# Performance work log

Hardware: AMD Instinct MI355X
Metric: run time of the kernel (lower is better)

Reference implementation:

```python
import jax, jax.numpy as jnp
import numpy as np

EPS = 1e-4
SLOPE = 0.01
NFFT = 512
HOP = 256
CH_IN = 8
CH_H = 64
FREQ = NFFT // 2 + 1
LEN = 48000
BATCH = 2


def hann(n):
    return (0.5 - 0.5 * jnp.cos(2.0 * np.pi * jnp.arange(n) / n)).astype(jnp.float32)


def stft(x):
    # x: (B, C, L) -> (B, 2, C, F, T)  (torch.stft: center=True, reflect pad, hann window)
    pad = NFFT // 2
    xp = jnp.pad(x, ((0, 0), (0, 0), (pad, pad)), mode='reflect')
    T = 1 + x.shape[-1] // HOP
    idx = jnp.arange(T)[:, None] * HOP + jnp.arange(NFFT)[None, :]
    frames = xp[..., idx] * hann(NFFT)            # (B, C, T, NFFT)
    sp = jnp.fft.rfft(frames, axis=-1)            # (B, C, T, F)
    sp = jnp.swapaxes(sp, -1, -2)                 # (B, C, F, T)
    return jnp.stack([sp.real, sp.imag], axis=1).astype(jnp.float32)


def istft(re, im, length):
    # re, im: (B, C, F, T) -> (B, C, length) via windowed overlap-add
    sp = jnp.swapaxes(re + 1j * im, -1, -2)       # (B, C, T, F)
    win = hann(NFFT)
    frames = jnp.fft.irfft(sp, n=NFFT, axis=-1) * win
    pad = NFFT // 2
    total = length + 2 * pad
    T = frames.shape[-2]
    idx = jnp.arange(T)[:, None] * HOP + jnp.arange(NFFT)[None, :]
    out = jnp.zeros(frames.shape[:-2] + (total,), frames.dtype).at[..., idx].add(frames)
    wsum = jnp.zeros((total,), frames.dtype).at[idx].add(jnp.broadcast_to(win ** 2, (T, NFFT)))
    return (out / jnp.maximum(wsum, 1e-11))[..., pad:pad + length]


def conv2d(x, w, b, padT=0):
    y = jax.lax.conv_general_dilated(x, w, (1, 1), ((0, 0), (padT, padT)),
                                     dimension_numbers=('NCHW', 'OIHW', 'NCHW'))
    return y + b[None, :, None, None]


def cconv(x, w, b, padT=0):
    # complex conv on x: (B,2,C,F,T); w: (2,O,C,kf,kt) = [W_real, W_imag]; b: (2,O)
    r = conv2d(x[:, 0], w[0], b[0], padT) - conv2d(x[:, 1], w[1], b[1], padT)
    i = conv2d(x[:, 1], w[0], b[0], padT) + conv2d(x[:, 0], w[1], b[1], padT)
    return jnp.stack([r, i], axis=1)


def modExp(x, m=5.0):
    em = float(np.exp(m))
    return jnp.where(x > m, (x - m) * em + em, jnp.exp(jnp.minimum(x, m)))


def cExp(t):
    e = modExp(t[:, 0]) - 1.0
    return jnp.stack([e * jnp.cos(t[:, 1] - 1.0), e * jnp.sin(t[:, 1] - 1.0)], axis=1)


def snap(x):
    x = jnp.where((x >= 0) & (x < EPS), EPS, x)
    return jnp.where((x < 0) & (x > -EPS), -EPS, x)


def cLog(t):
    re = snap(t[:, 0])
    im = snap(t[:, 1])
    real = jnp.log(jnp.sqrt(im ** 2 + re ** 2 + EPS ** 2) + 1.0)
    imag = jnp.arctan(im / re)
    return jnp.stack([real, imag], axis=1)


def cMul(a, b):
    r = a[:, 0] * b[:, 0] - a[:, 1] * b[:, 1]
    i = a[:, 0] * b[:, 1] + a[:, 1] * b[:, 0]
    return jnp.stack([r, i], axis=1)


def trelu(t, tr, b):
    nr = t[:, 0] * tr[0, 0] + t[:, 1] * tr[0, 1] + b[0]
    ni = t[:, 0] * tr[1, 0] + t[:, 1] * tr[1, 1] + b[1]
    return jnp.stack([jax.nn.leaky_relu(nr, SLOPE), jax.nn.leaky_relu(ni, SLOPE)], axis=1)


def tgate(t, tr, b):
    gr = jax.nn.sigmoid(t[:, 0] * tr[0, 0] + t[:, 1] * tr[0, 1] + b[0])
    gi = jax.nn.sigmoid(t[:, 0] * tr[1, 0] + t[:, 1] * tr[1, 1] + b[1])
    return gr * gi + (1.0 - gr) * (1.0 - gi)


def perm(t):
    return jnp.transpose(t, (0, 1, 3, 2, 4))


def lrelu(x):
    return jax.nn.leaky_relu(x, SLOPE)


def forward(mix, fs_w, fs_b, fr_w, fr_b, c1r_w, c1r_b, c1i_w, c1i_b, c1_w, c1_b,
            c2r_w, c2r_b, c2i_w, c2i_b, c2_w, c2_b, a1_t, a1_b, a2_t, a2_b,
            c3r_w, c3r_b, c3i_w, c3i_b, c3_w, c3_b, c4r_w, c4r_b, c4i_w, c4i_b,
            c4_w, c4_b, a3_t, a3_b, a4_t, a4_b, f1_w, f1_b, f2_w, f2_b,
            cw_w, cw_b, fg_t, fg_b):
    ts = perm(cconv(perm(stft(mix)), fs_w, fs_b))      # (B,2,C,F,T)
    # ---- branch 1 ----
    tl = cLog(ts)
    tl = jnp.stack([conv2d(tl[:, 0], c1r_w, c1r_b), conv2d(tl[:, 1], c1r_w, c1r_b)], 1)
    tl = jnp.stack([conv2d(lrelu(tl[:, 0]), c1i_w, c1i_b), conv2d(tl[:, 1], c1i_w, c1i_b)], 1)
    tl = trelu(cExp(tl), a1_t, a1_b)
    t = cconv(tl, c1_w, c1_b)
    tl = cLog(t)
    tl = jnp.stack([conv2d(tl[:, 0], c2r_w, c2r_b, 7), conv2d(tl[:, 1], c2r_w, c2r_b, 7)], 1)[..., :-7]
    tl = jnp.stack([conv2d(lrelu(tl[:, 0]), c2i_w, c2i_b, 7), conv2d(tl[:, 1], c2i_w, c2i_b, 7)], 1)[..., :-7]
    tl = cExp(tl)
    tl1 = tl
    tc = cconv(ts, c2_w, c2_b, 7)[..., :-7]
    t = trelu(cMul(tl, tc), a2_t, a2_b)
    t = cconv(t, f1_w, f1_b)
    td1 = jnp.sum(ts - t, axis=2, keepdims=True) / ts.shape[2]
    # ---- branch 2 ----
    tl = cLog(ts)
    tl = jnp.stack([conv2d(tl[:, 0], c3r_w, c3r_b), conv2d(tl[:, 1], c3r_w, c3r_b)], 1)
    tl = jnp.stack([conv2d(lrelu(tl[:, 0]), c3i_w, c3i_b), conv2d(tl[:, 1], c3i_w, c3i_b)], 1)
    tl = trelu(cExp(tl), a3_t, a3_b)
    t = cconv(tl, c3_w, c3_b)
    tl = cLog(t)
    tl = jnp.stack([conv2d(tl[:, 0], c4r_w, c4r_b, 7), conv2d(tl[:, 1], c4r_w, c4r_b, 7)], 1)[..., :-7]
    tl = jnp.stack([conv2d(lrelu(tl[:, 0]), c4i_w, c4i_b, 7), conv2d(tl[:, 1], c4i_w, c4i_b, 7)], 1)[..., :-7]
    tl = cExp(tl)
    tc = cconv(ts, c4_w, c4_b, 7)[..., :-7]
    t = trelu(cMul(tl, tc), a4_t, a4_b)
    td2 = cconv(t, f2_w, f2_b)                         # (B,2,1,F,T)
    # ---- fuse ----
    f = cconv(jnp.concatenate([tl1, tl], axis=2), cw_w, cw_b)
    f = tgate(f, fg_t, fg_b)[:, None]                  # (B,1,1,F,T)
    td = td1 * f + td2 * (1.0 - f)
    t = perm(cconv(perm(td), fr_w, fr_b))
    return istft(t[:, 0], t[:, 1], LEN)                # (B,1,LEN)


def setup_inputs() -> dict:
    ks = iter(jax.random.split(jax.random.key(0), 64))
    def rn(shape, s=0.05):
        return s * jax.random.normal(next(ks), shape, jnp.float32)
    F, C, H = FREQ, CH_IN, CH_H
    inp = {
        'mix': jax.random.normal(next(ks), (BATCH, C, LEN), jnp.float32),
        'fs_w': rn((2, F, F, 1, 1)), 'fs_b': rn((2, F), 0.01),
        'fr_w': rn((2, F, F, 1, 1)), 'fr_b': rn((2, F), 0.01),
        'c1r_w': rn((H, C, 1, 1)), 'c1r_b': rn((H,), 0.01),
        'c1i_w': rn((H, H, 1, 1)), 'c1i_b': rn((H,), 0.01),
        'c1_w': rn((2, H, H, 1, 1)), 'c1_b': rn((2, H), 0.01),
        'c2r_w': rn((H, H, 1, 8)), 'c2r_b': rn((H,), 0.01),
        'c2i_w': rn((H, H, 1, 8)), 'c2i_b': rn((H,), 0.01),
        'c2_w': rn((2, H, C, 1, 8)), 'c2_b': rn((2, H), 0.01),
        'a1_t': rn((2, 2, H, F, 1), 0.5), 'a1_b': rn((2, H, F, 1), 0.5),
        'a2_t': rn((2, 2, H, F, 1), 0.5), 'a2_b': rn((2, H, F, 1), 0.5),
        'c3r_w': rn((H, C, 1, 1)), 'c3r_b': rn((H,), 0.01),
        'c3i_w': rn((H, H, 1, 1)), 'c3i_b': rn((H,), 0.01),
        'c3_w': rn((2, H, H, 1, 1)), 'c3_b': rn((2, H), 0.01),
        'c4r_w': rn((H, H, 1, 8)), 'c4r_b': rn((H,), 0.01),
        'c4i_w': rn((H, H, 1, 8)), 'c4i_b': rn((H,), 0.01),
        'c4_w': rn((2, H, C, 1, 8)), 'c4_b': rn((2, H), 0.01),
        'a3_t': rn((2, 2, H, F, 1), 0.5), 'a3_b': rn((2, H, F, 1), 0.5),
        'a4_t': rn((2, 2, H, F, 1), 0.5), 'a4_b': rn((2, H, F, 1), 0.5),
        'f1_w': rn((2, C, H, 1, 1)), 'f1_b': rn((2, C), 0.01),
        'f2_w': rn((2, 1, H, 1, 1)), 'f2_b': rn((2, 1), 0.01),
        'cw_w': rn((2, 1, 2 * H, 1, 1)), 'cw_b': rn((2, 1), 0.01),
        'fg_t': rn((2, 2, 1, F, 1), 0.5), 'fg_b': rn((2, 1, F, 1), 0.5),
    }
    return inp


def reference(mix, fs_w, fs_b, fr_w, fr_b, c1r_w, c1r_b, c1i_w, c1i_b, c1_w, c1_b,
              c2r_w, c2r_b, c2i_w, c2i_b, c2_w, c2_b, a1_t, a1_b, a2_t, a2_b,
              c3r_w, c3r_b, c3i_w, c3i_b, c3_w, c3_b, c4r_w, c4r_b, c4i_w, c4i_b,
              c4_w, c4_b, a3_t, a3_b, a4_t, a4_b, f1_w, f1_b, f2_w, f2_b,
              cw_w, cw_b, fg_t, fg_b):
    return forward(mix, fs_w, fs_b, fr_w, fr_b, c1r_w, c1r_b, c1i_w, c1i_b, c1_w, c1_b,
                   c2r_w, c2r_b, c2i_w, c2i_b, c2_w, c2_b, a1_t, a1_b, a2_t, a2_b,
                   c3r_w, c3r_b, c3i_w, c3i_b, c3_w, c3_b, c4r_w, c4r_b, c4i_w, c4i_b,
                   c4_w, c4_b, a3_t, a3_b, a4_t, a4_b, f1_w, f1_b, f2_w, f2_b,
                   cw_w, cw_b, fg_t, fg_b)
```

## Files before the change

kernel.cpp:

```cpp
#include <hip/hip_runtime.h>
#include <math.h>

#define DEV __device__ __forceinline__

constexpr int B_   = 2;
constexpr int C_IN = 8;
constexpr int H_   = 64;
constexpr int F_   = 257;
constexpr int T_   = 188;
constexpr int TW   = 96;
constexpr int NFFT = 512;
constexpr int HOP  = 256;
constexpr int LEN  = 48000;
constexpr int PADL = 256;
constexpr int FT   = F_ * T_;
constexpr float EPSV  = 1e-4f;
constexpr float SLOPEV = 0.01f;
constexpr float PI2 = 6.283185307179586f;

typedef __attribute__((ext_vector_type(8))) short short8;
typedef __attribute__((ext_vector_type(4))) float float4v;

DEV float lrelu_f(float x) { return x > 0.f ? x : SLOPEV * x; }
DEV float snap_f(float x) {
  if (x >= 0.f && x < EPSV) return EPSV;
  if (x < 0.f && x > -EPSV) return -EPSV;
  return x;
}
DEV float modexp_f(float x) {
  const float em = 148.4131591025766f;
  return x > 5.f ? (x - 5.f) * em + em : expf(x);
}
DEV void cexp_f(float tr, float ti, float& er, float& ei) {
  float e = modexp_f(tr) - 1.f;
  float s, c;
  sincosf(ti - 1.f, &s, &c);
  er = e * c; ei = e * s;
}
DEV float sigmoid_f(float x) { return 1.f / (1.f + expf(-x)); }

DEV short f2bf(float x) {
  unsigned u = __float_as_uint(x);
  unsigned r = (u + 0x7fffu + ((u >> 16) & 1u)) >> 16;
  return (short)r;
}
DEV float bf2f(short h) {
  return __uint_as_float(((unsigned)(unsigned short)h) << 16);
}

__global__ __launch_bounds__(320) void k_stft(const float* __restrict__ mix,
                                              float* __restrict__ out) {
  __shared__ float xw[NFFT], xu[256], xv[256];
  int blk = blockIdx.x;
  int t = blk % T_;
  int bc = blk / T_;
  int c = bc % C_IN;
  int b = bc / C_IN;
  int tid = threadIdx.x;
  for (int n = tid; n < NFFT; n += 320) {
    int g = t * HOP + n - PADL;
    if (g < 0) g = -g;
    if (g >= LEN) g = 2 * LEN - 2 - g;
    float win = 0.5f - 0.5f * cosf((PI2 / NFFT) * n);
    xw[n] = mix[(b * C_IN + c) * LEN + g] * win;
  }
  __syncthreads();
  for (int n = tid + 1; n < 256; n += 320) {
    xu[n] = xw[n] + xw[NFFT - n];
    xv[n] = xw[n] - xw[NFFT - n];
  }
  __syncthreads();
  int f = tid;
  if (f < F_) {
    float sd, cd;
    sincosf((PI2 / NFFT) * f, &sd, &cd);
    float cs = cd, sn = sd, re = 0.f, im = 0.f;
    for (int n = 1; n < 256; ++n) {
      re += xu[n] * cs;
      im -= xv[n] * sn;
      float t2 = cs * cd - sn * sd;
      sn = sn * cd + cs * sd;
      cs = t2;
    }
    re += xw[0] + xw[256] * (1.f - 2.f * (f & 1));
    out[((b * 2 + 0) * C_IN + c) * FT + f * T_ + t] = re;
    out[((b * 2 + 1) * C_IN + c) * FT + f * T_ + t] = im;
  }
}

template<int CH>
__global__ void k_fmix(const float* __restrict__ X, const float* __restrict__ W,
                       const float* __restrict__ bias, float* __restrict__ Y) {
  int fo = blockIdx.x;
  int bc = blockIdx.y; int c = bc % CH; int b = bc / CH;
  int t = threadIdx.x;
  if (t >= T_) return;
  const float* wr = W + fo * F_;
  const float* wi = W + F_ * F_ + fo * F_;
  const float* xr = X + ((b * 2 + 0) * CH + c) * FT + t;
  const float* xi = X + ((b * 2 + 1) * CH + c) * FT + t;
  float ar = 0.f, ai = 0.f;
  for (int fi = 0; fi < F_; ++fi) {
    float wrv = wr[fi], wiv = wi[fi];
    float xrv = xr[fi * T_], xiv = xi[fi * T_];
    ar += wrv * xrv - wiv * xiv;
    ai += wrv * xiv + wiv * xrv;
  }
  float br = bias[fo], bi = bias[F_ + fo];
  Y[((b * 2 + 0) * CH + c) * FT + fo * T_ + t] = ar + br - bi;
  Y[((b * 2 + 1) * CH + c) * FT + fo * T_ + t] = ai + br + bi;
}

template<int CIN, int K>
DEV void repack_real_body(const float* __restrict__ W, short* __restrict__ wpk, int i) {
  constexpr int CC = (CIN >= 32) ? (CIN / 32) : 1;
  constexpr int NSTEP = (CIN * K + 31) / 32;
  int total = 2 * NSTEP * 4 * 64 * 8;
  if (i >= total) return;
  int j = i & 7;
  int lane = (i >> 3) & 63;
  int mt = (i >> 9) & 3;
  int s = (i >> 11) % NSTEP;
  int split = i / (NSTEP * 2048);
  int q = lane >> 4;
  int m = mt * 16 + (lane & 15);
  int tap = s / CC;
  int c = (s % CC) * 32 + q * 8 + j;
  float w = 0.f;
  if (c < CIN && tap < K) w = W[(m * CIN + c) * K + tap];
  short hi = f2bf(w);
  wpk[i] = split ? f2bf(w - bf2f(hi)) : hi;
}

template<int CIN2, int COUT2, int K>
DEV void repack_cplx_body(const float* __restrict__ W, short* __restrict__ wpk, int i) {
  constexpr int CIN = CIN2 / 2, COUT = COUT2 / 2;
  constexpr int NSTEP = CIN2 * K / 32;
  constexpr int MT = (COUT2 + 15) / 16;
  int total = 2 * NSTEP * MT * 64 * 8;
  if (i >= total) return;
  int j = i & 7;
  int lane = (i >> 3) & 63;
  int idx = i >> 9;
  int mt = idx % MT; idx /= MT;
  int s = idx % NSTEP;
  int split = idx / NSTEP;
  int q = lane >> 4;
  int m = mt * 16 + (lane & 15);
  int tap, pi, ci;
  if constexpr (CIN2 == 128) {
    tap = 0;
    int cs = s * 32 + q * 8 + j;
    int half = cs / 64, r = cs % 64;
    ci = half * 32 + r / 2;
    pi = r & 1;
  } else {
    tap = s * 2 + (q >> 1);
    int cs = (q & 1) * 8 + j;
    pi = cs / CIN;
    ci = cs % CIN;
  }
  float w = 0.f;
  if (m < COUT2) {
    int po = m / COUT, ho = m % COUT;
    float wr = W[((0 * COUT + ho) * CIN + ci) * K + tap];
    float wi = W[((1 * COUT + ho) * CIN + ci) * K + tap];
    w = (po == pi) ? wr : (po == 0 ? -wi : wi);
  }
  short hi = f2bf(w);
  wpk[i] = split ? f2bf(w - bf2f(hi)) : hi;
}

__global__ __launch_bounds__(256) void k_repack_all(
    const float* c1r_w, const float* c1i_w, const float* c2r_w, const float* c2i_w,
    const float* c3r_w, const float* c3i_w, const float* c4r_w, const float* c4i_w,
    const float* c1_w, const float* c2_w, const float* c3_w, const float* c4_w,
    const float* f1_w, const float* f2_w,
    short* o0, short* o1, short* o2, short* o3, short* o4, short* o5, short* o6,
    short* o7, short* o8, short* o9, short* o10, short* o11, short* o12, short* o13) {
  int i = blockIdx.x * 256 + threadIdx.x;
  switch (blockIdx.y) {
    case 0:  repack_real_body<C_IN, 1>(c1r_w, o0, i); break;
    case 1:  repack_real_body<H_,   1>(c1i_w, o1, i); break;
    case 2:  repack_real_body<H_,   8>(c2r_w, o2, i); break;
    case 3:  repack_real_body<H_,   8>(c2i_w, o3, i); break;
    case 4:  repack_real_body<C_IN, 1>(c3r_w, o4, i); break;
    case 5:  repack_real_body<H_,   1>(c3i_w, o5, i); break;
    case 6:  repack_real_body<H_,   8>(c4r_w, o6, i); break;
    case 7:  repack_real_body<H_,   8>(c4i_w, o7, i); break;
    case 8:  repack_cplx_body<128, 128, 1>(c1_w, o8, i); break;
    case 9:  repack_cplx_body<16,  128, 8>(c2_w, o9, i); break;
    case 10: repack_cplx_body<128, 128, 1>(c3_w, o10, i); break;
    case 11: repack_cplx_body<16,  128, 8>(c4_w, o11, i); break;
    case 12: repack_cplx_body<128, 16,  1>(f1_w, o12, i); break;
    case 13: repack_cplx_body<128, 2,   1>(f2_w, o13, i); break;
  }
}

template<int CIN, int K, int PRO>
__global__ __launch_bounds__(256) void k_conv_mfma(
    const float* __restrict__ X, const short* __restrict__ wpk,
    const float* __restrict__ bias, float* __restrict__ Y) {
  constexpr int CC = (CIN >= 32) ? (CIN / 32) : 1;
  constexpr int NSTEP = (CIN * K + 31) / 32;
  constexpr int PITCH = 72;
  constexpr int ROWS = TW + (K - 1);
  __shared__ short xs_hi[ROWS * PITCH];
  __shared__ short xs_lo[ROWS * PITCH];
  int f = blockIdx.x;
  int bp = blockIdx.y; int p = bp & 1; int b = bp >> 1;
  int t0 = blockIdx.z * TW;
  int tid = threadIdx.x;

  for (int i = tid; i < ROWS * PITCH; i += 256) { xs_hi[i] = 0; xs_lo[i] = 0; }
  __syncthreads();

  const float* Xr_ = X + (size_t)((b * 2 + 0) * CIN) * FT + f * T_;
  const float* Xi_ = X + (size_t)((b * 2 + 1) * CIN) * FT + f * T_;
  const float* Xp  = X + (size_t)((b * 2 + p) * CIN) * FT + f * T_;
  for (int i = tid; i < CIN * ROWS; i += 256) {
    int c = i / ROWS, rr = i % ROWS;
    int t = t0 + rr - (K - 1);
    if (t < 0 || t >= T_) continue;
    float v;
    if (PRO == 2) {
      float re = snap_f(Xr_[c * FT + t]);
      float im = snap_f(Xi_[c * FT + t]);
      v = (p == 0) ? logf(sqrtf(im * im + re * re + EPSV * EPSV) + 1.f)
                   : atanf(im / re);
    } else {
      v = Xp[c * FT + t];
      if (PRO == 1 && p == 0) v = lrelu_f(v);
    }
    short hi = f2bf(v);
    short lo = f2bf(v - bf2f(hi));
    xs_hi[rr * PITCH + c] = hi;
    xs_lo[rr * PITCH + c] = lo;
  }
  __syncthreads();

  int lane = tid & 63;
  int wv = __builtin_amdgcn_readfirstlane(tid >> 6);
  int mh = wv >> 1;
  int tc = wv & 1;
  int q = lane >> 4;
  int n = lane & 15;
  int wbase = tc * 48;

  float4v acc[2][3];
  #pragma unroll
  for (int mt = 0; mt < 2; ++mt)
    #pragma unroll
    for (int nt = 0; nt < 3; ++nt) acc[mt][nt] = (float4v)(0.f);

  const short8* wp = (const short8*)wpk;
  for (int s = 0; s < NSTEP; ++s) {
    int tap = s / CC;
    int c0 = (s % CC) * 32;
    short8 Bh[3], Bl[3];
    #pragma unroll
    for (int nt = 0; nt < 3; ++nt) {
      int off = (wbase + nt * 16 + n + tap) * PITCH + c0 + q * 8;
      Bh[nt] = *(const short8*)&xs_hi[off];
      Bl[nt] = *(const short8*)&xs_lo[off];
    }
    #pragma unroll
    for (int mt = 0; mt < 2; ++mt) {
      int mtg = mh * 2 + mt;
      short8 Ah = wp[((0 * NSTEP + s) * 4 + mtg) * 64 + lane];
      short8 Al = wp[((1 * NSTEP + s) * 4 + mtg) * 64 + lane];
      #pragma unroll
      for (int nt = 0; nt < 3; ++nt) {
        acc[mt][nt] = __builtin_amdgcn_mfma_f32_16x16x32_bf16(Ah, Bh[nt], acc[mt][nt], 0, 0, 0);
        acc[mt][nt] = __builtin_amdgcn_mfma_f32_16x16x32_bf16(Ah, Bl[nt], acc[mt][nt], 0, 0, 0);
        acc[mt][nt] = __builtin_amdgcn_mfma_f32_16x16x32_bf16(Al, Bh[nt], acc[mt][nt], 0, 0, 0);
      }
    }
  }

  float* Yp = Y + (size_t)((b * 2 + p) * H_) * FT + f * T_;
  #pragma unroll
  for (int nt = 0; nt < 3; ++nt) {
    int t = t0 + wbase + nt * 16 + n;
    if (t >= T_) continue;
    #pragma unroll
    for (int mt = 0; mt < 2; ++mt) {
      #pragma unroll
      for (int r = 0; r < 4; ++r) {
        int h = (mh * 2 + mt) * 16 + q * 4 + r;
        Yp[h * FT + t] = acc[mt][nt][r] + bias[h];
      }
    }
  }
}

template<int COUT2, int PRO>
__global__ __launch_bounds__(256) void k_cconv128(
    const float* __restrict__ X0, const float* __restrict__ X1,
    const short* __restrict__ wpk,
    const float* __restrict__ at, const float* __restrict__ ab,
    const float* __restrict__ bias, float* __restrict__ Y) {
  constexpr int MT = (COUT2 + 15) / 16;
  constexpr int MTW = (MT > 4) ? 4 : MT;
  constexpr int COUT = COUT2 / 2;
  constexpr int NSTEP = 4;
  constexpr int PITCH = 72;
  __shared__ short xs_hi[TW * PITCH];
  __shared__ short xs_lo[TW * PITCH];
  __shared__ float coef[6][64];
  int f = blockIdx.x;
  int b = blockIdx.y;
  int t0 = blockIdx.z * TW;
  int tid = threadIdx.x;
  int lane = tid & 63;
  int wv = __builtin_amdgcn_readfirstlane(tid >> 6);
  int mh = wv >> 1;
  int tc = wv & 1;
  int q = lane >> 4;
  int n = lane & 15;
  int wbase = tc * 48;

  if (tid < 64) {
    int h = tid;
    coef[0][h] = at[(0 * H_ + h) * F_ + f];
    coef[1][h] = at[(1 * H_ + h) * F_ + f];
    coef[2][h] = at[(2 * H_ + h) * F_ + f];
    coef[3][h] = at[(3 * H_ + h) * F_ + f];
    coef[4][h] = ab[h * F_ + f];
    coef[5][h] = ab[(H_ + h) * F_ + f];
  }
  for (int i = tid; i < TW * PITCH; i += 256) { xs_hi[i] = 0; xs_lo[i] = 0; }

  const float* b0r = X0 + (size_t)((b * 2 + 0) * H_) * FT + f * T_;
  const float* b0i = X0 + (size_t)((b * 2 + 1) * H_) * FT + f * T_;
  const float* b1r = X1 + (size_t)((b * 2 + 0) * H_) * FT + f * T_;
  const float* b1i = X1 + (size_t)((b * 2 + 1) * H_) * FT + f * T_;

  float4v acc[MTW][3];
  #pragma unroll
  for (int mt = 0; mt < MTW; ++mt)
    #pragma unroll
    for (int nt = 0; nt < 3; ++nt) acc[mt][nt] = (float4v)(0.f);

  const short8* wp = (const short8*)wpk;
  for (int half = 0; half < 2; ++half) {
    __syncthreads();
    for (int i = tid; i < 32 * TW; i += 256) {
      int hh = i / TW, tl = i % TW;
      int t = t0 + tl;
      if (t >= T_) continue;
      int h = half * 32 + hh;
      float xr = b0r[h * FT + t], xi = b0i[h * FT + t];
      float vr, vi;
      if (PRO == 1) {
        float er, ei;
        cexp_f(xr, xi, er, ei);
        vr = lrelu_f(er * coef[0][h] + ei * coef[1][h] + coef[4][h]);
        vi = lrelu_f(er * coef[2][h] + ei * coef[3][h] + coef[5][h]);
      } else {
        float yr = b1r[h * FT + t], yi = b1i[h * FT + t];
        float mr = xr * yr - xi * yi;
        float mi = xr * yi + xi * yr;
        vr = lrelu_f(mr * coef[0][h] + mi * coef[1][h] + coef[4][h]);
        vi = lrelu_f(mr * coef[2][h] + mi * coef[3][h] + coef[5][h]);
      }
      int cs0 = hh * 2, cs1 = hh * 2 + 1;
      short hr = f2bf(vr), hi2 = f2bf(vi);
      xs_hi[tl * PITCH + cs0] = hr;
      xs_lo[tl * PITCH + cs0] = f2bf(vr - bf2f(hr));
      xs_hi[tl * PITCH + cs1] = hi2;
      xs_lo[tl * PITCH + cs1] = f2bf(vi - bf2f(hi2));
    }
    __syncthreads();
    #pragma unroll
    for (int s2 = 0; s2 < 2; ++s2) {
      int s = half * 2 + s2;
      short8 Bh[3], Bl[3];
      #pragma unroll
      for (int nt = 0; nt < 3; ++nt) {
        int off = (wbase + nt * 16 + n) * PITCH + s2 * 32 + q * 8;
        Bh[nt] = *(const short8*)&xs_hi[off];
        Bl[nt] = *(const short8*)&xs_lo[off];
      }
      #pragma unroll
      for (int mt = 0; mt < MTW; ++mt) {
        int mtg = mh * 4 + mt;
        if (mtg >= MT) continue;
        short8 Ah = wp[((0 * NSTEP + s) * MT + mtg) * 64 + lane];
        short8 Al = wp[((1 * NSTEP + s) * MT + mtg) * 64 + lane];
        #pragma unroll
        for (int nt = 0; nt < 3; ++nt) {
          acc[mt][nt] = __builtin_amdgcn_mfma_f32_16x16x32_bf16(Ah, Bh[nt], acc[mt][nt], 0, 0, 0);
          acc[mt][nt] = __builtin_amdgcn_mfma_f32_16x16x32_bf16(Ah, Bl[nt], acc[mt][nt], 0, 0, 0);
          acc[mt][nt] = __builtin_amdgcn_mfma_f32_16x16x32_bf16(Al, Bh[nt], acc[mt][nt], 0, 0, 0);
        }
      }
    }
  }

  float* Yp = Y + (size_t)b * COUT2 * FT + f * T_;
  #pragma unroll
  for (int nt = 0; nt < 3; ++nt) {
    int t = t0 + wbase + nt * 16 + n;
    if (t >= T_) continue;
    #pragma unroll
    for (int mt = 0; mt < MTW; ++mt) {
      int mtg = mh * 4 + mt;
      if (mtg >= MT) continue;
      #pragma unroll
      for (int r = 0; r < 4; ++r) {
        int o2 = mtg * 16 + q * 4 + r;
        if (o2 >= COUT2) continue;
        int po = o2 / COUT, ho = o2 % COUT;
        float br = bias[ho], bi = bias[COUT + ho];
        float badd = (po == 0) ? br - bi : br + bi;
        Yp[o2 * FT + t] = acc[mt][nt][r] + badd;
      }
    }
  }
}

__global__ __launch_bounds__(256) void k_cconv16(
    const float* __restrict__ X, const short* __restrict__ wpk,
    const float* __restrict__ bias, float* __restrict__ Y) {
  constexpr int MT = 8, NSTEP = 4, PITCH = 24, ROWS = TW + 7, COUT = 64, COUT2 = 128;
  __shared__ short xs_hi[ROWS * PITCH];
  __shared__ short xs_lo[ROWS * PITCH];
  int f = blockIdx.x;
  int b = blockIdx.y;
  int t0 = blockIdx.z * TW;
  int tid = threadIdx.x;

  for (int i = tid; i < ROWS * PITCH; i += 256) { xs_hi[i] = 0; xs_lo[i] = 0; }
  __syncthreads();

  const float* Xp = X + (size_t)b * 16 * FT + f * T_;
  for (int i = tid; i < 16 * ROWS; i += 256) {
    int c = i / ROWS, rr = i % ROWS;
    int t = t0 + rr - 7;
    if (t < 0 || t >= T_) continue;
    float v = Xp[c * FT + t];
    short hi = f2bf(v);
    short lo = f2bf(v - bf2f(hi));
    xs_hi[rr * PITCH + c] = hi;
    xs_lo[rr * PITCH + c] = lo;
  }
  __syncthreads();

  int lane = tid & 63;
  int wv = __builtin_amdgcn_readfirstlane(tid >> 6);
  int mh = wv >> 1;
  int tc = wv & 1;
  int q = lane >> 4;
  int n = lane & 15;
  int wbase = tc * 48;

  float4v acc[4][3];
  #pragma unroll
  for (int mt = 0; mt < 4; ++mt)
    #pragma unroll
    for (int nt = 0; nt < 3; ++nt) acc[mt][nt] = (float4v)(0.f);

  const short8* wp = (const short8*)wpk;
  #pragma unroll
  for (int s = 0; s < NSTEP; ++s) {
    int tap = s * 2 + (q >> 1);
    int coff = (q & 1) * 8;
    short8 Bh[3], Bl[3];
    #pragma unroll
    for (int nt = 0; nt < 3; ++nt) {
      int off = (wbase + nt * 16 + n + tap) * PITCH + coff;
      Bh[nt] = *(const short8*)&xs_hi[off];
      Bl[nt] = *(const short8*)&xs_lo[off];
    }
    #pragma unroll
    for (int mt = 0; mt < 4; ++mt) {
      int mtg = mh * 4 + mt;
      short8 Ah = wp[((0 * NSTEP + s) * MT + mtg) * 64 + lane];
      short8 Al = wp[((1 * NSTEP + s) * MT + mtg) * 64 + lane];
      #pragma unroll
      for (int nt = 0; nt < 3; ++nt) {
        acc[mt][nt] = __builtin_amdgcn_mfma_f32_16x16x32_bf16(Ah, Bh[nt], acc[mt][nt], 0, 0, 0);
        acc[mt][nt] = __builtin_amdgcn_mfma_f32_16x16x32_bf16(Ah, Bl[nt], acc[mt][nt], 0, 0, 0);
        acc[mt][nt] = __builtin_amdgcn_mfma_f32_16x16x32_bf16(Al, Bh[nt], acc[mt][nt], 0, 0, 0);
      }
    }
  }

  float* Yp = Y + (size_t)b * COUT2 * FT + f * T_;
  #pragma unroll
  for (int nt = 0; nt < 3; ++nt) {
    int t = t0 + wbase + nt * 16 + n;
    if (t >= T_) continue;
    #pragma unroll
    for (int mt = 0; mt < 4; ++mt) {
      #pragma unroll
      for (int r = 0; r < 4; ++r) {
        int o2 = (mh * 4 + mt) * 16 + q * 4 + r;
        int po = o2 / COUT, ho = o2 % COUT;
        float br = bias[ho], bi = bias[COUT + ho];
        float badd = (po == 0) ? br - bi : br + bi;
        Yp[o2 * FT + t] = acc[mt][nt][r] + badd;
      }
    }
  }
}

__global__ void k_cexp(const float* __restrict__ X, float* __restrict__ Y) {
  int i = blockIdx.x * blockDim.x + threadIdx.x;
  if (i >= B_ * H_ * FT) return;
  int b = i / (H_ * FT);
  int r = i % (H_ * FT);
  int i0 = (b * 2) * H_ * FT + r;
  int i1 = i0 + H_ * FT;
  float er, ei;
  cexp_f(X[i0], X[i1], er, ei);
  Y[i0] = er;
  Y[i1] = ei;
}

__global__ void k_td1(const float* __restrict__ ts, const float* __restrict__ t8,
                      float* __restrict__ td1) {
  int i = blockIdx.x * blockDim.x + threadIdx.x;
  if (i >= B_ * 2 * FT) return;
  int bp = i / FT; int r = i % FT;
  const float* a = ts + bp * C_IN * FT + r;
  const float* c2 = t8 + bp * C_IN * FT + r;
  float acc = 0.f;
  #pragma unroll
  for (int c = 0; c < C_IN; ++c) acc += a[c * FT] - c2[c * FT];
  td1[i] = acc * (1.f / C_IN);
}

__global__ void k_fuse(const float* __restrict__ tl1, const float* __restrict__ tl2,
                       const float* __restrict__ td1, const float* __restrict__ td2,
                       const float* __restrict__ cw, const float* __restrict__ cwb,
                       const float* __restrict__ fgt, const float* __restrict__ fgb,
                       float* __restrict__ td) {
  int i = blockIdx.x * blockDim.x + threadIdx.x;
  if (i >= B_ * FT) return;
  int b = i / FT; int r = i % FT; int f = r / T_;
  const float* x1r = tl1 + (b * 2) * H_ * FT + r;
  const float* x1i = x1r + H_ * FT;
  const float* x2r = tl2 + (b * 2) * H_ * FT + r;
  const float* x2i = x2r + H_ * FT;
  float fr = 0.f, fi = 0.f;
  for (int c = 0; c < H_; ++c) {
    float w1r = cw[c], w2r = cw[H_ + c], w1i = cw[2 * H_ + c], w2i = cw[3 * H_ + c];
    float a1r = x1r[c * FT], a1i = x1i[c * FT];
    float a2r = x2r[c * FT], a2i = x2i[c * FT];
    fr += w1r * a1r - w1i * a1i + w2r * a2r - w2i * a2i;
    fi += w1r * a1i + w1i * a1r + w2r * a2i + w2i * a2r;
  }
  fr += cwb[0] - cwb[1];
  fi += cwb[0] + cwb[1];
  float t00 = fgt[f], t01 = fgt[F_ + f], t10 = fgt[2 * F_ + f], t11 = fgt[3 * F_ + f];
  float gr = sigmoid_f(fr * t00 + fi * t01 + fgb[f]);
  float gi = sigmoid_f(fr * t10 + fi * t11 + fgb[F_ + f]);
  float gg = gr * gi + (1.f - gr) * (1.f - gi);
  int i0 = (b * 2) * FT + r, i1 = i0 + FT;
  td[i0] = td1[i0] * gg + td2[i0] * (1.f - gg);
  td[i1] = td1[i1] * gg + td2[i1] * (1.f - gg);
}

__global__ __launch_bounds__(320) void k_iframes(const float* __restrict__ sp,
                                                 float* __restrict__ frames) {
  __shared__ float Xr[F_], Xi[F_];
  int blk = blockIdx.x;
  int t = blk % T_;
  int b = blk / T_;
  int tid = threadIdx.x;
  for (int i = tid; i < F_; i += 320) {
    Xr[i] = sp[(b * 2 + 0) * FT + i * T_ + t];
    Xi[i] = sp[(b * 2 + 1) * FT + i * T_ + t];
  }
  __syncthreads();
  int n = tid;
  if (n <= 256) {
    float sd, cd;
    sincosf((PI2 / NFFT) * n, &sd, &cd);
    float cs = cd, sn = sd;
    float ac = 0.f, as = 0.f;
    for (int f = 1; f < 256; ++f) {
      ac += Xr[f] * cs;
      as += Xi[f] * sn;
      float t2 = cs * cd - sn * sd;
      sn = sn * cd + cs * sd;
      cs = t2;
    }
    float base = Xr[0] + Xr[256] * (1.f - 2.f * (n & 1));
    float win = 0.5f - 0.5f * cd;
    float scale = win * (1.f / NFFT);
    float* fr = frames + (size_t)(b * T_ + t) * NFFT;
    fr[n] = (base + 2.f * ac - 2.f * as) * scale;
    if (n >= 1 && n <= 255)
      fr[NFFT - n] = (base + 2.f * ac + 2.f * as) * scale;
  }
}

__global__ void k_ola(const float* __restrict__ frames, float* __restrict__ out) {
  int i = blockIdx.x * blockDim.x + threadIdx.x;
  if (i >= B_ * LEN) return;
  int b = i / LEN; int j = i % LEN;
  int p = j + PADL;
  int t0 = p / HOP; int n0 = p - t0 * HOP;
  float acc = 0.f, wsum = 0.f;
  if (t0 < T_) {
    acc += frames[(b * T_ + t0) * NFFT + n0];
    float w = 0.5f - 0.5f * cosf((PI2 / NFFT) * n0);
    wsum += w * w;
  }
  int t1 = t0 - 1, n1 = n0 + HOP;
  if (t1 >= 0 && t1 < T_) {
    acc += frames[(b * T_ + t1) * NFFT + n1];
    float w = 0.5f - 0.5f * cosf((PI2 / NFFT) * n1);
    wsum += w * w;
  }
  out[i] = acc / fmaxf(wsum, 1e-11f);
}

extern "C" void kernel_launch(void* const* d_in, const int* in_sizes, int n_in,
                              void* d_out, int out_size, void* d_ws, size_t ws_size,
                              hipStream_t stream) {
  const float* mix   = (const float*)d_in[0];
  const float* fs_w  = (const float*)d_in[1];
  const float* fs_b  = (const float*)d_in[2];
  const float* fr_w  = (const float*)d_in[3];
  const float* fr_b  = (const float*)d_in[4];
  const float* c1r_w = (const float*)d_in[5];
  const float* c1r_b = (const float*)d_in[6];
  const float* c1i_w = (const float*)d_in[7];
  const float* c1i_b = (const float*)d_in[8];
  const float* c1_w  = (const float*)d_in[9];
  const float* c1_b  = (const float*)d_in[10];
  const float* c2r_w = (const float*)d_in[11];
  const float* c2r_b = (const float*)d_in[12];
  const float* c2i_w = (const float*)d_in[13];
  const float* c2i_b = (const float*)d_in[14];
  const float* c2_w  = (const float*)d_in[15];
  const float* c2_b  = (const float*)d_in[16];
  const float* a1_t  = (const float*)d_in[17];
  const float* a1_b  = (const float*)d_in[18];
  const float* a2_t  = (const float*)d_in[19];
  const float* a2_b  = (const float*)d_in[20];
  const float* c3r_w = (const float*)d_in[21];
  const float* c3r_b = (const float*)d_in[22];
  const float* c3i_w = (const float*)d_in[23];
  const float* c3i_b = (const float*)d_in[24];
  const float* c3_w  = (const float*)d_in[25];
  const float* c3_b  = (const float*)d_in[26];
  const float* c4r_w = (const float*)d_in[27];
  const float* c4r_b = (const float*)d_in[28];
  const float* c4i_w = (const float*)d_in[29];
  const float* c4i_b = (const float*)d_in[30];
  const float* c4_w  = (const float*)d_in[31];
  const float* c4_b  = (const float*)d_in[32];
  const float* a3_t  = (const float*)d_in[33];
  const float* a3_b  = (const float*)d_in[34];
  const float* a4_t  = (const float*)d_in[35];
  const float* a4_b  = (const float*)d_in[36];
  const float* f1_w  = (const float*)d_in[37];
  const float* f1_b  = (const float*)d_in[38];
  const float* f2_w  = (const float*)d_in[39];
  const float* f2_b  = (const float*)d_in[40];
  const float* cw_w  = (const float*)d_in[41];
  const float* cw_b  = (const float*)d_in[42];
  const float* fg_t  = (const float*)d_in[43];
  const float* fg_b  = (const float*)d_in[44];

  const size_t S8 = (size_t)B_ * 2 * C_IN * FT;
  const size_t SH = (size_t)B_ * 2 * H_ * FT;
  const size_t S1 = (size_t)B_ * 2 * FT;
  float* ws  = (float*)d_ws;
  float* ts0 = ws;
  float* ts  = ts0 + S8;
  float* A   = ts + S8;
  float* Bb  = A + SH;
  float* Cc  = Bb + SH;
  float* td1 = Cc + SH;
  float* td2 = td1 + S1;
  float* tdf = td2 + S1;
  float* tdr = tdf + S1;
  float* s8  = ts0;
  float* frames = ts0;

  short* wtail = (short*)(tdr + S1);
  constexpr int SZ_C8K1   = 2 * 1  * 4 * 64 * 8;
  constexpr int SZ_C64K1  = 2 * 2  * 4 * 64 * 8;
  constexpr int SZ_C64K8  = 2 * 16 * 4 * 64 * 8;
  constexpr int SZ_CC128  = 2 * 4  * 8 * 64 * 8;
  constexpr int SZ_CF     = 2 * 4  * 1 * 64 * 8;
  short* w_c1r = wtail;
  short* w_c1i = w_c1r + SZ_C8K1;
  short* w_c2r = w_c1i + SZ_C64K1;
  short* w_c2i = w_c2r + SZ_C64K8;
  short* w_c3r = w_c2i + SZ_C64K8;
  short* w_c3i = w_c3r + SZ_C8K1;
  short* w_c4r = w_c3i + SZ_C64K1;
  short* w_c4i = w_c4r + SZ_C64K8;
  short* w_cc1 = w_c4i + SZ_C64K8;
  short* w_cc2 = w_cc1 + SZ_CC128;
  short* w_cc3 = w_cc2 + SZ_CC128;
  short* w_cc4 = w_cc3 + SZ_CC128;
  short* w_cf1 = w_cc4 + SZ_CC128;
  short* w_cf2 = w_cf1 + SZ_CF;

  const int nH = B_ * H_ * FT;
  const int nP = B_ * FT;
  const dim3 rgrid(F_, B_ * 2, 2);
  const dim3 cgrid(F_, B_, 2);

  k_repack_all<<<dim3(256, 14), 256, 0, stream>>>(
      c1r_w, c1i_w, c2r_w, c2i_w, c3r_w, c3i_w, c4r_w, c4i_w,
      c1_w, c2_w, c3_w, c4_w, f1_w, f2_w,
      w_c1r, w_c1i, w_c2r, w_c2i, w_c3r, w_c3i, w_c4r, w_c4i,
      w_cc1, w_cc2, w_cc3, w_cc4, w_cf1, w_cf2);

  k_stft<<<B_ * C_IN * T_, 320, 0, stream>>>(mix, ts0);
  k_fmix<C_IN><<<dim3(F_, B_ * C_IN), 192, 0, stream>>>(ts0, fs_w, fs_b, ts);

  k_conv_mfma<C_IN, 1, 2><<<rgrid, 256, 0, stream>>>(ts, w_c1r, c1r_b, A);
  k_conv_mfma<H_, 1, 1><<<rgrid, 256, 0, stream>>>(A, w_c1i, c1i_b, Bb);
  k_cconv128<128, 1><<<cgrid, 256, 0, stream>>>(Bb, Bb, w_cc1, a1_t, a1_b, c1_b, A);
  k_conv_mfma<H_, 8, 2><<<rgrid, 256, 0, stream>>>(A, w_c2r, c2r_b, Bb);
  k_conv_mfma<H_, 8, 1><<<rgrid, 256, 0, stream>>>(Bb, w_c2i, c2i_b, A);
  k_cexp<<<(nH + 255) / 256, 256, 0, stream>>>(A, Bb);
  k_cconv16<<<cgrid, 256, 0, stream>>>(ts, w_cc2, c2_b, A);
  k_cconv128<16, 2><<<cgrid, 256, 0, stream>>>(Bb, A, w_cf1, a2_t, a2_b, f1_b, s8);
  k_td1<<<(B_ * 2 * FT + 255) / 256, 256, 0, stream>>>(ts, s8, td1);

  k_conv_mfma<C_IN, 1, 2><<<rgrid, 256, 0, stream>>>(ts, w_c3r, c3r_b, A);
  k_conv_mfma<H_, 1, 1><<<rgrid, 256, 0, stream>>>(A, w_c3i, c3i_b, Cc);
  k_cconv128<128, 1><<<cgrid, 256, 0, stream>>>(Cc, Cc, w_cc3, a3_t, a3_b, c3_b, A);
  k_conv_mfma<H_, 8, 2><<<rgrid, 256, 0, stream>>>(A, w_c4r, c4r_b, Cc);
  k_conv_mfma<H_, 8, 1><<<rgrid, 256, 0, stream>>>(Cc, w_c4i, c4i_b, A);
  k_cexp<<<(nH + 255) / 256, 256, 0, stream>>>(A, Cc);
  k_cconv16<<<cgrid, 256, 0, stream>>>(ts, w_cc4, c4_b, A);
  k_cconv128<2, 2><<<cgrid, 256, 0, stream>>>(Cc, A, w_cf2, a4_t, a4_b, f2_b, td2);

  k_fuse<<<(nP + 255) / 256, 256, 0, stream>>>(Bb, Cc, td1, td2, cw_w, cw_b, fg_t, fg_b, tdf);
  k_fmix<1><<<dim3(F_, B_), 192, 0, stream>>>(tdf, fr_w, fr_b, tdr);
  k_iframes<<<B_ * T_, 320, 0, stream>>>(tdr, frames);
  k_ola<<<(B_ * LEN + 255) / 256, 256, 0, stream>>>(frames, (float*)d_out);
}
```

Baseline: 942.5 us.

## Register-block frequency mixing over eight outputs and fold td1 into fuse kernel

```diff
diff --git a/kernel.cpp b/kernel.cpp
--- a/kernel.cpp
+++ b/kernel.cpp
@@ -88,27 +88,52 @@
   }
 }
 
+__global__ __launch_bounds__(256) void k_wt(const float* __restrict__ fs_w,
+                                            const float* __restrict__ fr_w,
+                                            float* __restrict__ wt_fs,
+                                            float* __restrict__ wt_fr) {
+  int i = blockIdx.x * 256 + threadIdx.x;
+  if (i >= 2 * F_ * F_) return;
+  const float* W = blockIdx.y ? fr_w : fs_w;
+  float* O = blockIdx.y ? wt_fr : wt_fs;
+  int p = i / (F_ * F_); int rem = i % (F_ * F_);
+  int fi = rem / F_; int fo = rem % F_;
+  O[i] = W[p * F_ * F_ + fo * F_ + fi];
+}
+
 template<int CH>
-__global__ void k_fmix(const float* __restrict__ X, const float* __restrict__ W,
-                       const float* __restrict__ bias, float* __restrict__ Y) {
-  int fo = blockIdx.x;
+__global__ __launch_bounds__(192) void k_fmix2(const float* __restrict__ X,
+                                               const float* __restrict__ WT,
+                                               const float* __restrict__ bias,
+                                               float* __restrict__ Y) {
+  int fo0 = blockIdx.x * 8;
   int bc = blockIdx.y; int c = bc % CH; int b = bc / CH;
   int t = threadIdx.x;
   if (t >= T_) return;
-  const float* wr = W + fo * F_;
-  const float* wi = W + F_ * F_ + fo * F_;
   const float* xr = X + ((b * 2 + 0) * CH + c) * FT + t;
   const float* xi = X + ((b * 2 + 1) * CH + c) * FT + t;
-  float ar = 0.f, ai = 0.f;
+  float ar[8] = {0.f, 0.f, 0.f, 0.f, 0.f, 0.f, 0.f, 0.f};
+  float ai[8] = {0.f, 0.f, 0.f, 0.f, 0.f, 0.f, 0.f, 0.f};
   for (int fi = 0; fi < F_; ++fi) {
-    float wrv = wr[fi], wiv = wi[fi];
     float xrv = xr[fi * T_], xiv = xi[fi * T_];
-    ar += wrv * xrv - wiv * xiv;
-    ai += wrv * xiv + wiv * xrv;
-  }
-  float br = bias[fo], bi = bias[F_ + fo];
-  Y[((b * 2 + 0) * CH + c) * FT + fo * T_ + t] = ar + br - bi;
-  Y[((b * 2 + 1) * CH + c) * FT + fo * T_ + t] = ai + br + bi;
+    const float* wr = WT + fi * F_ + fo0;
+    const float* wi = WT + F_ * F_ + fi * F_ + fo0;
+    #pragma unroll
+    for (int k = 0; k < 8; ++k) {
+      float wrv = wr[k], wiv = wi[k];
+      ar[k] += wrv * xrv - wiv * xiv;
+      ai[k] += wrv * xiv + wiv * xrv;
+    }
+  }
+  #pragma unroll
+  for (int k = 0; k < 8; ++k) {
+    int fo = fo0 + k;
+    if (fo < F_) {
+      float br = bias[fo], bi = bias[F_ + fo];
+      Y[((b * 2 + 0) * CH + c) * FT + fo * T_ + t] = ar[k] + br - bi;
+      Y[((b * 2 + 1) * CH + c) * FT + fo * T_ + t] = ai[k] + br + bi;
+    }
+  }
 }
 
 template<int CIN, int K>
@@ -519,27 +544,27 @@
   Y[i1] = ei;
 }
 
-__global__ void k_td1(const float* __restrict__ ts, const float* __restrict__ t8,
-                      float* __restrict__ td1) {
-  int i = blockIdx.x * blockDim.x + threadIdx.x;
-  if (i >= B_ * 2 * FT) return;
-  int bp = i / FT; int r = i % FT;
-  const float* a = ts + bp * C_IN * FT + r;
-  const float* c2 = t8 + bp * C_IN * FT + r;
-  float acc = 0.f;
-  #pragma unroll
-  for (int c = 0; c < C_IN; ++c) acc += a[c * FT] - c2[c * FT];
-  td1[i] = acc * (1.f / C_IN);
-}
-
 __global__ void k_fuse(const float* __restrict__ tl1, const float* __restrict__ tl2,
-                       const float* __restrict__ td1, const float* __restrict__ td2,
+                       const float* __restrict__ ts, const float* __restrict__ s8,
+                       const float* __restrict__ td2,
                        const float* __restrict__ cw, const float* __restrict__ cwb,
                        const float* __restrict__ fgt, const float* __restrict__ fgb,
                        float* __restrict__ td) {
   int i = blockIdx.x * blockDim.x + threadIdx.x;
   if (i >= B_ * FT) return;
   int b = i / FT; int r = i % FT; int f = r / T_;
+  float t1r = 0.f, t1i = 0.f;
+  {
+    const float* a0 = ts + (size_t)(b * 16) * FT + r;
+    const float* c0 = s8 + (size_t)(b * 16) * FT + r;
+    #pragma unroll
+    for (int c = 0; c < C_IN; ++c) {
+      t1r += a0[c * FT] - c0[c * FT];
+      t1i += a0[(C_IN + c) * FT] - c0[(C_IN + c) * FT];
+    }
+    t1r *= (1.f / C_IN);
+    t1i *= (1.f / C_IN);
+  }
   const float* x1r = tl1 + (b * 2) * H_ * FT + r;
   const float* x1i = x1r + H_ * FT;
   const float* x2r = tl2 + (b * 2) * H_ * FT + r;
@@ -559,8 +584,8 @@
   float gi = sigmoid_f(fr * t10 + fi * t11 + fgb[F_ + f]);
   float gg = gr * gi + (1.f - gr) * (1.f - gi);
   int i0 = (b * 2) * FT + r, i1 = i0 + FT;
-  td[i0] = td1[i0] * gg + td2[i0] * (1.f - gg);
-  td[i1] = td1[i1] * gg + td2[i1] * (1.f - gg);
+  td[i0] = t1r * gg + td2[i0] * (1.f - gg);
+  td[i1] = t1i * gg + td2[i1] * (1.f - gg);
 }
 
 __global__ __launch_bounds__(320) void k_iframes(const float* __restrict__ sp,
@@ -677,14 +702,13 @@
   float* A   = ts + S8;
   float* Bb  = A + SH;
   float* Cc  = Bb + SH;
-  float* td1 = Cc + SH;
-  float* td2 = td1 + S1;
+  float* td2 = Cc + SH;
   float* tdf = td2 + S1;
   float* tdr = tdf + S1;
-  float* s8  = ts0;
+  float* s8  = tdr + S1;
   float* frames = ts0;
 
-  short* wtail = (short*)(tdr + S1);
+  short* wtail = (short*)(s8 + S8);
   constexpr int SZ_C8K1   = 2 * 1  * 4 * 64 * 8;
   constexpr int SZ_C64K1  = 2 * 2  * 4 * 64 * 8;
   constexpr int SZ_C64K8  = 2 * 16 * 4 * 64 * 8;
@@ -704,6 +728,8 @@
   short* w_cc4 = w_cc3 + SZ_CC128;
   short* w_cf1 = w_cc4 + SZ_CC128;
   short* w_cf2 = w_cf1 + SZ_CF;
+  float* wt_fs = (float*)(w_cf2 + SZ_CF);
+  float* wt_fr = wt_fs + 2 * F_ * F_;
 
   const int nH = B_ * H_ * FT;
   const int nP = B_ * FT;
@@ -715,9 +741,10 @@
       c1_w, c2_w, c3_w, c4_w, f1_w, f2_w,
       w_c1r, w_c1i, w_c2r, w_c2i, w_c3r, w_c3i, w_c4r, w_c4i,
       w_cc1, w_cc2, w_cc3, w_cc4, w_cf1, w_cf2);
+  k_wt<<<dim3((2 * F_ * F_ + 255) / 256, 2), 256, 0, stream>>>(fs_w, fr_w, wt_fs, wt_fr);
 
   k_stft<<<B_ * C_IN * T_, 320, 0, stream>>>(mix, ts0);
-  k_fmix<C_IN><<<dim3(F_, B_ * C_IN), 192, 0, stream>>>(ts0, fs_w, fs_b, ts);
+  k_fmix2<C_IN><<<dim3(33, B_ * C_IN), 192, 0, stream>>>(ts0, wt_fs, fs_b, ts);
 
   k_conv_mfma<C_IN, 1, 2><<<rgrid, 256, 0, stream>>>(ts, w_c1r, c1r_b, A);
   k_conv_mfma<H_, 1, 1><<<rgrid, 256, 0, stream>>>(A, w_c1i, c1i_b, Bb);
@@ -727,7 +754,6 @@
   k_cexp<<<(nH + 255) / 256, 256, 0, stream>>>(A, Bb);
   k_cconv16<<<cgrid, 256, 0, stream>>>(ts, w_cc2, c2_b, A);
   k_cconv128<16, 2><<<cgrid, 256, 0, stream>>>(Bb, A, w_cf1, a2_t, a2_b, f1_b, s8);
-  k_td1<<<(B_ * 2 * FT + 255) / 256, 256, 0, stream>>>(ts, s8, td1);
 
   k_conv_mfma<C_IN, 1, 2><<<rgrid, 256, 0, stream>>>(ts, w_c3r, c3r_b, A);
   k_conv_mfma<H_, 1, 1><<<rgrid, 256, 0, stream>>>(A, w_c3i, c3i_b, Cc);
@@ -738,8 +764,8 @@
   k_cconv16<<<cgrid, 256, 0, stream>>>(ts, w_cc4, c4_b, A);
   k_cconv128<2, 2><<<cgrid, 256, 0, stream>>>(Cc, A, w_cf2, a4_t, a4_b, f2_b, td2);
 
-  k_fuse<<<(nP + 255) / 256, 256, 0, stream>>>(Bb, Cc, td1, td2, cw_w, cw_b, fg_t, fg_b, tdf);
-  k_fmix<1><<<dim3(F_, B_), 192, 0, stream>>>(tdf, fr_w, fr_b, tdr);
+  k_fuse<<<(nP + 255) / 256, 256, 0, stream>>>(Bb, Cc, ts, s8, td2, cw_w, cw_b, fg_t, fg_b, tdf);
+  k_fmix2<1><<<dim3(33, B_), 192, 0, stream>>>(tdf, wt_fr, fr_b, tdr);
   k_iframes<<<B_ * T_, 320, 0, stream>>>(tdr, frames);
   k_ola<<<(B_ * LEN + 255) / 256, 256, 0, stream>>>(frames, (float*)d_out);
 }
```

Result: slower. 1.035 ms (+9.8%).
